# Kernel tuning notes

Measured on AMD Instinct MI355X. Metric: run time of the kernel, lower is better.

The kernel has to match this reference:

```python
import jax, jax.numpy as jnp
import numpy as np
from jax import lax


def conv1x1(x, w, b):
    # x [B,Ci,H,W], w [Co,Ci], b [Co]
    return jnp.einsum('oi,bihw->bohw', w, x) + b[None, :, None, None]


def dil_conv_relu(x, w, b):
    # 3x3 conv, dilation 2, padding 2 (make_layers with dilation=True), then ReLU
    y = lax.conv_general_dilated(x, w, (1, 1), [(2, 2), (2, 2)], rhs_dilation=(2, 2),
                                 dimension_numbers=('NCHW', 'OIHW', 'NCHW'))
    return jax.nn.relu(y + b[None, :, None, None])


def conv1d_relu(x, w, b):
    # x [n,c,L], w [o,i,9], padding 4 -> same length; conv + ReLU (nn.Sequential(Conv2d, ReLU))
    y = lax.conv_general_dilated(x, w, (1,), [(4, 4)], dimension_numbers=('NCH', 'OIH', 'NCH'))
    return jax.nn.relu(y + b[None, :, None])


def dulr_pass(slices, w, b):
    # slices [L,n,c,m]; out[0]=slices[0]; out[i]=convrelu(out[i-1]) + slices[i]
    def step(carry, s):
        new = conv1d_relu(carry, w, b) + s
        return new, new
    _, rest = lax.scan(step, slices[0], slices[1:])
    return jnp.concatenate([slices[:1], rest], axis=0)


def conv_du(x, w, b):
    # down pass then up pass over rows (kernel (1,9) -> 1D conv along width)
    rows = jnp.moveaxis(x, 2, 0)            # [h,n,c,w]
    rows = dulr_pass(rows, w, b)
    rows = dulr_pass(rows[::-1], w, b)[::-1]
    return jnp.moveaxis(rows, 0, 2)


def conv_lr(x, w, b):
    # left-right then right-left over columns (kernel (9,1) -> 1D conv along height)
    cols = jnp.moveaxis(x, 3, 0)            # [w,n,c,h]
    cols = dulr_pass(cols, w, b)
    cols = dulr_pass(cols[::-1], w, b)[::-1]
    return jnp.moveaxis(cols, 0, 3)


def setup_inputs() -> dict:
    key = jax.random.key(0)
    ks = jax.random.split(key, 24)
    B, H, W = 4, 64, 64
    std = 0.01
    f32 = jnp.float32
    d = {}
    d['in_data'] = jax.random.normal(ks[0], (B, 1025, H, W), f32)
    d['wA'] = jax.random.normal(ks[1], (128, 1024), f32) * std
    d['bA'] = jax.random.normal(ks[2], (128,), f32) * std
    d['wB'] = jax.random.normal(ks[3], (128, 1024), f32) * std
    d['bB'] = jax.random.normal(ks[4], (128,), f32) * std
    d['wC'] = jax.random.normal(ks[5], (1024, 1024), f32) * std
    d['bC'] = jax.random.normal(ks[6], (1024,), f32) * std
    d['gamma'] = jnp.array(0.1, f32)
    chans = [(512, 1024), (512, 512), (512, 512), (256, 512), (128, 256), (64, 128)]
    for i, (co, ci) in enumerate(chans):
        d[f'bw{i+1}'] = jax.random.normal(ks[7 + 2 * i], (co, ci, 3, 3), f32) * std
        d[f'bb{i+1}'] = jax.random.normal(ks[8 + 2 * i], (co,), f32) * std
    d['du_w'] = jax.random.normal(ks[19], (64, 64, 9), f32) * std
    d['du_b'] = jax.random.normal(ks[20], (64,), f32) * std
    d['lr_w'] = jax.random.normal(ks[21], (64, 64, 9), f32) * std
    d['lr_b'] = jax.random.normal(ks[22], (64,), f32) * std
    d['ow'] = jax.random.normal(ks[23], (1, 64), f32) * std
    d['ob'] = jnp.zeros((1,), f32)
    return d


def reference(in_data, wA, bA, wB, bB, wC, bC, gamma,
              bw1, bb1, bw2, bb2, bw3, bb3, bw4, bb4, bw5, bb5, bw6, bb6,
              du_w, du_b, lr_w, lr_b, ow, ob):
    x = in_data[:, :1024]                   # [B,1024,H,W]
    f = in_data[:, 1024:1025]               # [B,1,H,W]
    B, C, H, W = x.shape
    N = H * W
    # appearance_A(x) -> query [B,128,N]
    q = conv1x1(x, wA, bA).reshape(B, 128, N)
    # f1024 = f broadcast to 1024 channels; flow_B(f1024) (1x1 conv) == f * sum_i wB[:,i] + bB
    k = (f * wB.sum(axis=1)[None, :, None, None] + bB[None, :, None, None]).reshape(B, 128, N)
    energy = jnp.einsum('bcn,bcm->bnm', q, k)           # [B,N,N] = q^T k
    att = jax.nn.softmax(energy, axis=-1)
    v = conv1x1(x, wC, bC).reshape(B, C, N)             # appearance_C
    out = jnp.einsum('bcj,bij->bci', v, att).reshape(B, C, H, W)  # bmm(v, att^T)
    x = gamma * out + x
    for w_, b_ in ((bw1, bb1), (bw2, bb2), (bw3, bb3), (bw4, bb4), (bw5, bb5), (bw6, bb6)):
        x = dil_conv_relu(x, w_, b_)
    x = conv_du(x, du_w, du_b)
    x = conv_lr(x, lr_w, lr_b)
    x = jax.nn.relu(conv1x1(x, ow, ob))                 # o_layer
    # F.upsample(scale_factor=8) default nearest
    x = jnp.repeat(jnp.repeat(x, 8, axis=2), 8, axis=3)
    return x
```

## Files before the change

kernel.cpp:

```cpp
#include <hip/hip_runtime.h>


#define NPIX 4096

typedef _Float16 f16;
typedef _Float16 f16x8 __attribute__((ext_vector_type(8)));
typedef _Float16 f16x4 __attribute__((ext_vector_type(4)));
typedef float f32x4 __attribute__((ext_vector_type(4)));

__device__ inline void async16(const void* g, void* l) {
  __builtin_amdgcn_global_load_lds(
      (const __attribute__((address_space(1))) unsigned int*)g,
      (__attribute__((address_space(3))) unsigned int*)l, 16, 0, 0);
}


__global__ void rf_zero(float* __restrict__ z) { z[threadIdx.x] = 0.f; }

__global__ void rf_s(const float* __restrict__ wB, const float* __restrict__ bA,
                     float* __restrict__ s_out, float* __restrict__ c0_out) {
  int c = threadIdx.x;
  const float* row = wB + (size_t)c * 1024;
  float acc = 0.f;
  for (int i = 0; i < 1024; ++i) acc += row[i];
  s_out[c] = acc;
  __shared__ float sh[128];
  sh[c] = acc * bA[c];
  __syncthreads();
  for (int off = 64; off > 0; off >>= 1) {
    if (c < off) sh[c] += sh[c + off];
    __syncthreads();
  }
  if (c == 0) c0_out[0] = sh[0];
}

__global__ void rf_u(const float* __restrict__ wA, const float* __restrict__ s,
                     float* __restrict__ u) {
  int i = blockIdx.x * 256 + threadIdx.x;
  float acc = 0.f;
  for (int c = 0; c < 128; ++c) acc += s[c] * wA[(size_t)c * 1024 + i];
  u[i] = acc;
}

__global__ void rf_fstat(const float* __restrict__ in, float* __restrict__ fstat) {
  int b = blockIdx.x;
  int t = threadIdx.x;
  const float* f = in + ((size_t)b * 1025 + 1024) * NPIX;
  float mx = -1e30f, mn = 1e30f;
  for (int j = t; j < NPIX; j += 256) {
    float v = f[j];
    mx = fmaxf(mx, v);
    mn = fminf(mn, v);
  }
  __shared__ float smx[256], smn[256];
  smx[t] = mx; smn[t] = mn;
  __syncthreads();
  for (int off = 128; off > 0; off >>= 1) {
    if (t < off) {
      smx[t] = fmaxf(smx[t], smx[t + off]);
      smn[t] = fminf(smn[t], smn[t + off]);
    }
    __syncthreads();
  }
  if (t == 0) { fstat[b] = smx[0]; fstat[4 + b] = smn[0]; }
}

__global__ __launch_bounds__(256) void rf_A(const float* __restrict__ in,
                                            const float* __restrict__ u,
                                            const float* __restrict__ c0p,
                                            const float* __restrict__ fst,
                                            float* __restrict__ A, float* __restrict__ M) {
  __shared__ float ul[1024];
  int b = blockIdx.y;
  int n = blockIdx.x * 256 + threadIdx.x;
  for (int s = threadIdx.x; s < 1024; s += 256) ul[s] = u[s];
  __syncthreads();
  const float* xp = in + (size_t)b * 1025 * NPIX + n;
  float acc = c0p[0];
#pragma unroll 8
  for (int i = 0; i < 1024; ++i) acc = fmaf(ul[i], xp[(size_t)i * NPIX], acc);
  A[b * NPIX + n] = acc;
  M[b * NPIX + n] = fmaxf(acc * fst[b], acc * fst[4 + b]);
}

__global__ void rf_Z(const float* __restrict__ in, const float* __restrict__ A,
                     const float* __restrict__ M, float* __restrict__ iZ) {
  int idx = blockIdx.x * 4 + (threadIdx.x >> 6);
  int lane = threadIdx.x & 63;
  int b = idx >> 12;
  const float* f = in + ((size_t)b * 1025 + 1024) * NPIX;
  float a = A[idx], m = M[idx];
  float acc = 0.f;
#pragma unroll 4
  for (int it = 0; it < 64; ++it) acc += __expf(a * f[lane + it * 64] - m);
  for (int off = 32; off > 0; off >>= 1) acc += __shfl_down(acc, off, 64);
  if (lane == 0) iZ[idx] = 1.0f / acc;
}


__global__ void rf_xsplit(const float* __restrict__ in, f16* __restrict__ xh) {
  __shared__ float tl[64][65];
  int nt = blockIdx.x, ct = blockIdx.y, b = blockIdx.z;
  int n0 = nt * 64, c0 = ct * 64;
  int tid = threadIdx.x;
  for (int s = tid; s < 4096; s += 256) {
    int r = s >> 6, c = s & 63;
    tl[r][c] = in[((size_t)b * 1025 + c0 + r) * NPIX + n0 + c];
  }
  __syncthreads();
  for (int s = tid; s < 512; s += 256) {
    int n = s >> 3, g = s & 7;
    f16x8 hb;
#pragma unroll
    for (int q = 0; q < 8; ++q) hb[q] = (f16)(16.f * tl[g * 8 + q][n]);
    size_t o = ((size_t)b * NPIX + n0 + n) * 1024 + c0 + g * 8;
    *(f16x8*)&xh[o] = hb;
  }
}


__global__ void rf_wC1(const float* __restrict__ wC, f16* __restrict__ wh) {
  int base = (blockIdx.x * 256 + threadIdx.x) * 8;
  f16x8 hb;
#pragma unroll
  for (int q = 0; q < 8; ++q) hb[q] = (f16)(256.f * wC[base + q]);
  *(f16x8*)&wh[base] = hb;
}


__global__ __launch_bounds__(256, 2) void rf_vgemmm(
    const f16* __restrict__ wh, const f16* __restrict__ xh,
    const float* __restrict__ bC, f16* __restrict__ vH) {
  __shared__ f16 sA[2][4096], sB[2][4096];
  const int tid = threadIdx.x;
  const int nb = blockIdx.x * 128, cb = blockIdx.y * 128, b = blockIdx.z;
  const int pA = tid & 127;
  const int wv = tid >> 6, lane = tid & 63;
  const int mrow = lane & 15, quad = lane >> 4;
  const int wm = (wv & 1) * 64, wn = (wv >> 1) * 64;
  const size_t abase = (size_t)(cb + pA) * 1024;
  const size_t bbase = ((size_t)b * NPIX + nb + pA) * 1024;
  f32x4 acc[4][4];
#pragma unroll
  for (int i = 0; i < 4; ++i)
#pragma unroll
    for (int j = 0; j < 4; ++j) acc[i][j] = (f32x4){0.f, 0.f, 0.f, 0.f};

  auto stage = [&](int k0, int pb) {
#pragma unroll
    for (int s = 0; s < 2; ++s) {
      const int cc = ((tid + 256 * s) >> 7) & 3;
      const int lb = ((tid & ~63) + 256 * s) * 8;
      async16(wh + abase + k0 + cc * 8, &sA[pb][lb]);
      async16(xh + bbase + k0 + cc * 8, &sB[pb][lb]);
    }
  };
  stage(0, 0);
  int p = 0;
  for (int k0 = 0; k0 < 1024; k0 += 32) {
    __syncthreads();
    if (k0 + 32 < 1024) stage(k0 + 32, p ^ 1);
    f16x8 fa[4], fb[4];
#pragma unroll
    for (int mi = 0; mi < 4; ++mi)
      fa[mi] = *(const f16x8*)&sA[p][(quad * 128 + wm + mi * 16 + mrow) * 8];
#pragma unroll
    for (int ni = 0; ni < 4; ++ni)
      fb[ni] = *(const f16x8*)&sB[p][(quad * 128 + wn + ni * 16 + mrow) * 8];
#pragma unroll
    for (int mi = 0; mi < 4; ++mi)
#pragma unroll
      for (int ni = 0; ni < 4; ++ni)
        acc[mi][ni] = __builtin_amdgcn_mfma_f32_16x16x32_f16(fa[mi], fb[ni], acc[mi][ni], 0, 0, 0);
    p ^= 1;
  }
  const float inv = 1.0f / 4096.0f;
#pragma unroll
  for (int mi = 0; mi < 4; ++mi) {
#pragma unroll
    for (int rg = 0; rg < 4; ++rg) {
      int c = cb + wm + mi * 16 + quad * 4 + rg;
      float bv = bC[c];
#pragma unroll
      for (int ni = 0; ni < 4; ++ni) {
        int j = nb + wn + ni * 16 + mrow;
        vH[((size_t)b * 1024 + c) * NPIX + j] =
            (f16)(16.f * (acc[mi][ni][rg] * inv + bv));
      }
    }
  }
}


__global__ __launch_bounds__(256, 2) void rf_attm(
    const f16* __restrict__ vH,
    const float* __restrict__ Aarr, const float* __restrict__ Marr,
    const float* __restrict__ iZ, const float* __restrict__ in,
    const float* __restrict__ gptr, f16* __restrict__ yH) {
  __shared__ f16 sAh[3][8192];
  __shared__ f16 sPh[2][4096];
  __shared__ float fl[4096];
  const int tid = threadIdx.x;
  const int ib = blockIdx.x * 128, cb = blockIdx.y * 256, b = blockIdx.z;
  const int wv = tid >> 6, lane = tid & 63;
  const int mrow = lane & 15, quad = lane >> 4;
  const int wm = wv * 64;
  const int ni_ = tid & 127;
  const int kc0 = tid >> 7;
  const float av2 = Aarr[b * NPIX + ib + ni_] * 1.44269504f;
  const float mv2 = Marr[b * NPIX + ib + ni_] * 1.44269504f;
  const float* f = in + ((size_t)b * 1025 + 1024) * NPIX;
  const f16* vrow = vH + ((size_t)b * 1024 + cb + tid) * NPIX;

  f32x4 acc[4][8];
#pragma unroll
  for (int i = 0; i < 4; ++i)
#pragma unroll
    for (int j = 0; j < 8; ++j) acc[i][j] = (f32x4){0.f, 0.f, 0.f, 0.f};

  auto stage = [&](int j0, int pb) {
#pragma unroll
    for (int s = 0; s < 4; ++s)
      async16(vrow + j0 + s * 8, &sAh[pb][(s * 256 + tid) * 8]);
  };
  auto doP = [&](int j0, int pb) {
#pragma unroll
    for (int it = 0; it < 2; ++it) {
      const int kc = kc0 + 2 * it;
      const float4 fa4 = *(const float4*)&fl[j0 + kc * 8];
      const float4 fb4 = *(const float4*)&fl[j0 + kc * 8 + 4];
      const float fj[8] = {fa4.x, fa4.y, fa4.z, fa4.w, fb4.x, fb4.y, fb4.z, fb4.w};
      f16x8 ph;
#pragma unroll
      for (int q = 0; q < 8; ++q)
        ph[q] = (f16)exp2f(fmaf(av2, fj[q], -mv2));
      *(f16x8*)&sPh[pb][(kc * 128 + ni_) * 8] = ph;
    }
  };

#pragma unroll
  for (int s = 0; s < 4; ++s)
    async16(f + (tid + 256 * s) * 4, &fl[((tid & ~63) + 256 * s) * 4]);
  stage(0, 0);
  asm volatile("s_waitcnt vmcnt(0)" ::: "memory");
  __builtin_amdgcn_s_barrier();
  doP(0, 0);
  stage(32, 1);
  asm volatile("s_waitcnt lgkmcnt(0)" ::: "memory");
  __builtin_amdgcn_s_barrier();

  for (int k = 0; k < 126; ++k) {
    const int pa = k % 3;
    const int pp = k & 1;
    f16x8 fa[4], fb[8];
#pragma unroll
    for (int mi = 0; mi < 4; ++mi)
      fa[mi] = *(const f16x8*)&sAh[pa][(quad * 256 + wm + mi * 16 + mrow) * 8];
#pragma unroll
    for (int ni = 0; ni < 8; ++ni)
      fb[ni] = *(const f16x8*)&sPh[pp][(quad * 128 + ni * 16 + mrow) * 8];
    stage((k + 2) * 32, (k + 2) % 3);
    doP((k + 1) * 32, pp ^ 1);
#pragma unroll
    for (int mi = 0; mi < 4; ++mi)
#pragma unroll
      for (int ni = 0; ni < 8; ++ni)
        acc[mi][ni] = __builtin_amdgcn_mfma_f32_16x16x32_f16(fa[mi], fb[ni], acc[mi][ni], 0, 0, 0);
    asm volatile("s_waitcnt vmcnt(4) lgkmcnt(0)" ::: "memory");
    __builtin_amdgcn_s_barrier();
  }
  {
    f16x8 fa[4], fb[8];
#pragma unroll
    for (int mi = 0; mi < 4; ++mi)
      fa[mi] = *(const f16x8*)&sAh[0][(quad * 256 + wm + mi * 16 + mrow) * 8];
#pragma unroll
    for (int ni = 0; ni < 8; ++ni)
      fb[ni] = *(const f16x8*)&sPh[0][(quad * 128 + ni * 16 + mrow) * 8];
    doP(127 * 32, 1);
#pragma unroll
    for (int mi = 0; mi < 4; ++mi)
#pragma unroll
      for (int ni = 0; ni < 8; ++ni)
        acc[mi][ni] = __builtin_amdgcn_mfma_f32_16x16x32_f16(fa[mi], fb[ni], acc[mi][ni], 0, 0, 0);
    asm volatile("s_waitcnt vmcnt(0) lgkmcnt(0)" ::: "memory");
    __builtin_amdgcn_s_barrier();
  }
  {
    f16x8 fa[4], fb[8];
#pragma unroll
    for (int mi = 0; mi < 4; ++mi)
      fa[mi] = *(const f16x8*)&sAh[1][(quad * 256 + wm + mi * 16 + mrow) * 8];
#pragma unroll
    for (int ni = 0; ni < 8; ++ni)
      fb[ni] = *(const f16x8*)&sPh[1][(quad * 128 + ni * 16 + mrow) * 8];
#pragma unroll
    for (int mi = 0; mi < 4; ++mi)
#pragma unroll
      for (int ni = 0; ni < 8; ++ni)
        acc[mi][ni] = __builtin_amdgcn_mfma_f32_16x16x32_f16(fa[mi], fb[ni], acc[mi][ni], 0, 0, 0);
  }

  const float g = gptr[0];
  const float inv16 = 1.0f / 16.0f;
  float zvi[8];
#pragma unroll
  for (int ni = 0; ni < 8; ++ni)
    zvi[ni] = iZ[b * NPIX + ib + ni * 16 + mrow] * inv16;
#pragma unroll
  for (int mi = 0; mi < 4; ++mi) {
    const int cbase = cb + wm + mi * 16 + quad * 4;
#pragma unroll
    for (int ni = 0; ni < 8; ++ni) {
      const int i = ib + ni * 16 + mrow;
      f16x4 hv;
#pragma unroll
      for (int rg = 0; rg < 4; ++rg) {
        float xr = in[((size_t)b * 1025 + cbase + rg) * NPIX + i];
        hv[rg] = (f16)(16.f * (g * (acc[mi][ni][rg] * zvi[ni]) + xr));
      }
      *(f16x4*)&yH[((size_t)b * NPIX + i) * 1024 + cbase] = hv;
    }
  }
}


__global__ void rf_wfragc(const float* __restrict__ w, f16* __restrict__ F,
                          int CI, int CO) {
  int gid = blockIdx.x * 256 + threadIdx.x;
  const int C16 = CO >> 4, KI = CI >> 5;
  const int total = 9 * KI * C16 * 64;
  if (gid >= total) return;
  int lane = gid & 63;
  int rest = gid >> 6;
  int c16 = rest % C16;
  int rest2 = rest / C16;
  int k = rest2 % KI;
  int t = rest2 / KI;
  int co = c16 * 16 + (lane & 15);
  int ci = k * 32 + (lane >> 4) * 8;
  f16x8 hb;
#pragma unroll
  for (int j = 0; j < 8; ++j)
    hb[j] = (f16)(256.0f * w[((size_t)co * CI + ci + j) * 9 + t]);
  *(f16x8*)&F[(size_t)gid * 8] = hb;
}


template <int BM, int BN, bool F32OUT>
__global__ __launch_bounds__(256, 2) void rf_mconv(
    const f16* __restrict__ xh, const f16* __restrict__ F,
    const float* __restrict__ bias, const float* __restrict__ zp,
    f16* __restrict__ oh, float* __restrict__ of, int CI, int CO) {
  constexpr int ROWS = BM / 64;
  constexpr int TPI = 4096 / BM;
  constexpr int HROWS = ROWS + 4;
  constexpr int COLP = 72;
  constexpr int CHUNKS = HROWS * 4 * COLP;
  constexpr int NSTG = (CHUNKS + 255) / 256;
  __shared__ f16 sA[2][NSTG * 2048];
  const int tid = threadIdx.x;
  const int blkpx = blockIdx.x;
  const int cob = blockIdx.y * BN;
  const int b = blkpx / TPI;
  const int h0 = (blkpx - b * TPI) * ROWS;

  const int wv = tid >> 6, lane = tid & 63;
  const int mrow = lane & 15, quad = lane >> 4;
  const int wm = (BN == 128) ? (wv & 1) * 64 : wv * 64;
  const int wn = (BN == 128) ? (wv >> 1) * 64 : 0;
  const int r_out = wm >> 6;
  const int KI = CI >> 5;
  const int C16 = CO >> 4;
  const int cb16 = (cob + wn) >> 4;

  f32x4 acc[4][4];
#pragma unroll
  for (int i = 0; i < 4; ++i)
#pragma unroll
    for (int j = 0; j < 4; ++j) acc[i][j] = (f32x4){0.f, 0.f, 0.f, 0.f};

  const f16* abase[NSTG];
  unsigned vmask = 0;
#pragma unroll
  for (int s = 0; s < NSTG; ++s) {
    int idx = tid + 256 * s;
    int rowks = idx / COLP;
    int col = idx - rowks * COLP;
    int r = rowks >> 2, ks = rowks & 3;
    int srow = h0 + r - 2, scol = col - 2;
    bool ok = (idx < CHUNKS) && ((unsigned)srow < 64u) && ((unsigned)scol < 64u);
    abase[s] = ok ? xh + (((size_t)b * 64 + srow) * 64 + scol) * CI + ks * 8
                  : (const f16*)zp;
    if (ok) vmask |= (1u << s);
  }
  auto stageA = [&](int k, int pb) {
#pragma unroll
    for (int s = 0; s < NSTG; ++s) {
      const f16* sp = abase[s] + (((vmask >> s) & 1u) ? k * 32 : 0);
      async16(sp, &sA[pb][((tid & ~63) + 256 * s) * 8]);
    }
  };

  const f16* Fb = F + ((size_t)cb16 * 64 + lane) * 8;

  stageA(0, 0);
  int p = 0;
  for (int k = 0; k < KI; ++k) {
    __syncthreads();
    if (k + 1 < KI) stageA(k + 1, p ^ 1);
#pragma unroll
    for (int t = 0; t < 9; ++t) {
      const int dh = (t / 3) * 2 - 2, dw = (t - (t / 3) * 3) * 2 - 2;
      f16x8 fb[4];
#pragma unroll
      for (int ni = 0; ni < 4; ++ni)
        fb[ni] = *(const f16x8*)(Fb + ((size_t)(t * KI + k) * C16 + ni) * 512);
      f16x8 fa[4];
#pragma unroll
      for (int mi = 0; mi < 4; ++mi)
        fa[mi] = *(const f16x8*)&sA[p][(((r_out + dh + 2) * 4 + quad) * COLP +
                                       mi * 16 + mrow + dw + 2) * 8];
#pragma unroll
      for (int mi = 0; mi < 4; ++mi)
#pragma unroll
        for (int ni = 0; ni < 4; ++ni)
          acc[mi][ni] = __builtin_amdgcn_mfma_f32_16x16x32_f16(fa[mi], fb[ni], acc[mi][ni], 0, 0, 0);
    }
    p ^= 1;
  }

  const float inv = 1.0f / 4096.0f;
  float bvs[4];
#pragma unroll
  for (int ni = 0; ni < 4; ++ni) bvs[ni] = bias[cob + wn + ni * 16 + mrow];
#pragma unroll
  for (int mi = 0; mi < 4; ++mi) {
#pragma unroll
    for (int rg = 0; rg < 4; ++rg) {
      int px = wm + mi * 16 + quad * 4 + rg;
      int hh = h0 + (px >> 6), wwp = px & 63;
#pragma unroll
      for (int ni = 0; ni < 4; ++ni) {
        int co = cob + wn + ni * 16 + mrow;
        float vv = fmaxf(acc[mi][ni][rg] * inv + bvs[ni], 0.f);
        if (F32OUT) {
          of[(((size_t)b * CO + co) * 64 + hh) * 64 + wwp] = vv;
        } else {
          oh[(((size_t)b * 64 + hh) * 64 + wwp) * CO + co] = (f16)(vv * 16.f);
        }
      }
    }
  }
}


__global__ void rf_wfrag(const float* __restrict__ w, f16* __restrict__ fh) {
  int gid = blockIdx.x * 256 + threadIdx.x;
  if (gid >= 4608) return;
  int lane = gid & 63;
  int rem = gid >> 6;
  int kc = rem & 1;
  int rem2 = rem >> 1;
  int t = rem2 % 9;
  int w4 = rem2 / 9;
  int co = w4 * 16 + (lane & 15);
  int cib = kc * 32 + (lane >> 4) * 8;
  f16x8 hb;
#pragma unroll
  for (int j = 0; j < 8; ++j)
    hb[j] = (f16)(256.f * w[((size_t)co * 64 + cib + j) * 9 + t]);
  *(f16x8*)&fh[(size_t)gid * 8] = hb;
}


__global__ __launch_bounds__(256, 1) void rf_mscan(
    const float* __restrict__ src, float* __restrict__ dst,
    const f16* __restrict__ fh, const float* __restrict__ bias, int dir) {
  __shared__ f16 ch[72 * 64];
  const int b = blockIdx.x;
  const int tid = threadIdx.x;
  const int wave = tid >> 6, lane = tid & 63;
  const int quad = lane >> 4, l15 = lane & 15;

  f16x8 Ah[9][2];
#pragma unroll
  for (int t = 0; t < 9; ++t)
#pragma unroll
    for (int kc = 0; kc < 2; ++kc)
      Ah[t][kc] = *(const f16x8*)&fh[(((wave * 9 + t) * 2 + kc) * 64 + lane) * 8];
  float bvs[4];
#pragma unroll
  for (int r = 0; r < 4; ++r) bvs[r] = bias[wave * 16 + quad * 4 + r];

  for (int s = tid; s < 2304; s += 256) ((unsigned*)ch)[s] = 0u;
  __syncthreads();

  const size_t sbase = (size_t)b * 64 * 4096;
  const int row0 = (dir > 0) ? 0 : 63;
  {
    int pos0 = tid & 63, cig = tid >> 6;
#pragma unroll
    for (int q = 0; q < 16; ++q) {
      int ci = cig * 16 + q;
      float v = src[sbase + (size_t)ci * 4096 + row0 * 64 + pos0];
      dst[sbase + (size_t)ci * 4096 + row0 * 64 + pos0] = v;
      int rowIdx = pos0 + 4;
      ch[rowIdx * 64 + (((ci >> 3) ^ (rowIdx & 7)) << 3) + (ci & 7)] = (f16)v;
    }
  }
  __syncthreads();

  const float inv = 1.0f / 256.0f;
  for (int s = 1; s < 64; ++s) {
    const int row = (dir > 0) ? s : 63 - s;
    float srow[4][4];
#pragma unroll
    for (int nt = 0; nt < 4; ++nt)
#pragma unroll
      for (int r = 0; r < 4; ++r)
        srow[nt][r] = src[sbase + (size_t)(wave * 16 + quad * 4 + r) * 4096 +
                          row * 64 + nt * 16 + l15];
    f32x4 acc[4];
#pragma unroll
    for (int nt = 0; nt < 4; ++nt) acc[nt] = (f32x4){0.f, 0.f, 0.f, 0.f};
#pragma unroll
    for (int t = 0; t < 9; ++t)
#pragma unroll
      for (int kc = 0; kc < 2; ++kc) {
#pragma unroll
        for (int nt = 0; nt < 4; ++nt) {
          int rowIdx = nt * 16 + l15 + t;
          int gr = kc * 4 + quad;
          f16x8 Bh = *(const f16x8*)&ch[rowIdx * 64 + ((gr ^ (rowIdx & 7)) << 3)];
          acc[nt] = __builtin_amdgcn_mfma_f32_16x16x32_f16(Ah[t][kc], Bh, acc[nt], 0, 0, 0);
        }
      }
    __syncthreads();
#pragma unroll
    for (int nt = 0; nt < 4; ++nt) {
      int pos = nt * 16 + l15;
      int rowIdx = pos + 4;
      f16x4 hv;
#pragma unroll
      for (int r = 0; r < 4; ++r) {
        float v = fmaxf(acc[nt][r] * inv + bvs[r], 0.f) + srow[nt][r];
        dst[sbase + (size_t)(wave * 16 + quad * 4 + r) * 4096 + row * 64 + pos] = v;
        hv[r] = (f16)v;
      }
      int ci0 = wave * 16 + quad * 4;
      *(f16x4*)&ch[rowIdx * 64 + (((ci0 >> 3) ^ (rowIdx & 7)) << 3) + (ci0 & 7)] = hv;
    }
    __syncthreads();
  }
}


__global__ void rf_transpose(const float* __restrict__ src, float* __restrict__ dst) {
  int bc = blockIdx.x;
  __shared__ float tl[64][65];
  int tid = threadIdx.x;
  const float* sp = src + (size_t)bc * 4096;
  float* dp = dst + (size_t)bc * 4096;
  for (int s = tid; s < 4096; s += 256) {
    int h = s >> 6, w = s & 63;
    tl[w][h] = sp[s];
  }
  __syncthreads();
  for (int s = tid; s < 4096; s += 256) dp[s] = tl[s >> 6][s & 63];
}


__global__ void rf_final(const float* __restrict__ t, const float* __restrict__ ow,
                         const float* __restrict__ ob, float* __restrict__ out) {
  int b = blockIdx.y;
  int s = blockIdx.x * 256 + threadIdx.x;
  int w = s >> 6, h = s & 63;
  float acc = ob[0];
  for (int c = 0; c < 64; ++c)
    acc += ow[c] * t[(((size_t)b * 64 + c) * 64 + w) * 64 + h];
  acc = fmaxf(acc, 0.f);
  float4 vv = make_float4(acc, acc, acc, acc);
  for (int dy = 0; dy < 8; ++dy) {
    float* dp = out + ((size_t)b * 512 + h * 8 + dy) * 512 + w * 8;
    *(float4*)dp = vv;
    *(float4*)(dp + 4) = vv;
  }
}


extern "C" void kernel_launch(void* const* d_in, const int* in_sizes, int n_in,
                              void* d_out, int out_size, void* d_ws, size_t ws_size,
                              hipStream_t stream) {
  const float* in    = (const float*)d_in[0];
  const float* wA    = (const float*)d_in[1];
  const float* bA    = (const float*)d_in[2];
  const float* wB    = (const float*)d_in[3];
  const float* wC    = (const float*)d_in[5];
  const float* bC    = (const float*)d_in[6];
  const float* gamma = (const float*)d_in[7];
  const float* bw1 = (const float*)d_in[8];  const float* bb1 = (const float*)d_in[9];
  const float* bw2 = (const float*)d_in[10]; const float* bb2 = (const float*)d_in[11];
  const float* bw3 = (const float*)d_in[12]; const float* bb3 = (const float*)d_in[13];
  const float* bw4 = (const float*)d_in[14]; const float* bb4 = (const float*)d_in[15];
  const float* bw5 = (const float*)d_in[16]; const float* bb5 = (const float*)d_in[17];
  const float* bw6 = (const float*)d_in[18]; const float* bb6 = (const float*)d_in[19];
  const float* du_w = (const float*)d_in[20]; const float* du_b = (const float*)d_in[21];
  const float* lr_w = (const float*)d_in[22]; const float* lr_b = (const float*)d_in[23];
  const float* ow   = (const float*)d_in[24]; const float* ob   = (const float*)d_in[25];
  float* out = (float*)d_out;
  float* ws = (float*)d_ws;

  f16* vH  = (f16*)(ws + 0);
  f16* xTh = (f16*)(ws + 4194304);
  f16* wCh = (f16*)(ws + 8388608);
  f16* yH  = (f16*)(ws + 16777216);
  f16* w1h = (f16*)(ws + 0);
  f16* c1H = (f16*)(ws + 2359296);
  f16* w3h = (f16*)(ws + 6553600);
  f16* w2h = (f16*)(ws + 16777216);
  f16* c2H = (f16*)(ws + 17956864);
  f16* w4h = (f16*)(ws + 22151168);
  f16* c4H = (f16*)(ws + 22740992);
  f16* c3H = c1H;
  f16* w5h = (f16*)(ws + 0);
  f16* c5H = (f16*)(ws + 147456);
  f16* w6h = (f16*)(ws + 1196032);
  float* tin = ws + 1232896;
  float* t0  = ws + 2281472;
  float* t1  = ws + 3330048;
  f16* duFh = (f16*)(ws + 4378624);
  f16* lrFh = (f16*)(ws + 4397056);
  float* sm = ws + 33554432;
  float* A_  = sm;
  float* M_  = sm + 16384;
  float* iZ  = sm + 32768;
  float* u_  = sm + 49152;
  float* s_  = sm + 50176;
  float* c0_ = sm + 50304;
  float* fst = sm + 50308;
  float* zp  = sm + 50432;

  rf_zero<<<1, 64, 0, stream>>>(zp);
  rf_s<<<1, 128, 0, stream>>>(wB, bA, s_, c0_);
  rf_u<<<4, 256, 0, stream>>>(wA, s_, u_);
  rf_fstat<<<4, 256, 0, stream>>>(in, fst);
  rf_A<<<dim3(16, 4), 256, 0, stream>>>(in, u_, c0_, fst, A_, M_);
  rf_Z<<<4096, 256, 0, stream>>>(in, A_, M_, iZ);
  rf_xsplit<<<dim3(64, 16, 4), 256, 0, stream>>>(in, xTh);
  rf_wC1<<<512, 256, 0, stream>>>(wC, wCh);
  rf_vgemmm<<<dim3(32, 8, 4), 256, 0, stream>>>(wCh, xTh, bC, vH);
  rf_attm<<<dim3(32, 4, 4), 256, 0, stream>>>(vH, A_, M_, iZ, in, gamma, yH);

  rf_wfragc<<<2304, 256, 0, stream>>>(bw1, w1h, 1024, 512);
  rf_wfragc<<<1152, 256, 0, stream>>>(bw3, w3h, 512, 512);
  rf_mconv<128, 128, false><<<dim3(128, 4), 256, 0, stream>>>(
      yH, w1h, bb1, zp, c1H, nullptr, 1024, 512);
  rf_wfragc<<<1152, 256, 0, stream>>>(bw2, w2h, 512, 512);
  rf_wfragc<<<576, 256, 0, stream>>>(bw4, w4h, 512, 256);
  rf_wfragc<<<144, 256, 0, stream>>>(bw5, w5h, 256, 128);
  rf_wfragc<<<36, 256, 0, stream>>>(bw6, w6h, 128, 64);
  rf_mconv<128, 128, false><<<dim3(128, 4), 256, 0, stream>>>(
      c1H, w2h, bb2, zp, c2H, nullptr, 512, 512);
  rf_mconv<128, 128, false><<<dim3(128, 4), 256, 0, stream>>>(
      c2H, w3h, bb3, zp, c3H, nullptr, 512, 512);
  rf_mconv<128, 128, false><<<dim3(128, 2), 256, 0, stream>>>(
      c3H, w4h, bb4, zp, c4H, nullptr, 512, 256);
  rf_wfrag<<<18, 256, 0, stream>>>(du_w, duFh);
  rf_wfrag<<<18, 256, 0, stream>>>(lr_w, lrFh);
  rf_mconv<128, 128, false><<<dim3(128, 1), 256, 0, stream>>>(
      c4H, w5h, bb5, zp, c5H, nullptr, 256, 128);
  rf_mconv<256, 64, true><<<dim3(64, 1), 256, 0, stream>>>(
      c5H, w6h, bb6, zp, nullptr, tin, 128, 64);

  rf_mscan<<<4, 256, 0, stream>>>(tin, t0, duFh, du_b, +1);
  rf_mscan<<<4, 256, 0, stream>>>(t0, t1, duFh, du_b, -1);
  rf_transpose<<<256, 256, 0, stream>>>(t1, t0);
  rf_mscan<<<4, 256, 0, stream>>>(t0, t1, lrFh, lr_b, +1);
  rf_mscan<<<4, 256, 0, stream>>>(t1, t0, lrFh, lr_b, -1);
  rf_final<<<dim3(16, 4), 256, 0, stream>>>(t0, ow, ob, out);
}
```

Before: 1.683 ms.

## Prefetch conv weight fragments one tap ahead and remap blocks across XCDs

The dilated-conv MFMA kernel now double-buffers its global weight-fragment loads in registers, loading the next tap's fragments while the current tap's MFMAs run. It also moves the activation staging for the next K-step to after the compute, and unrolls the K loop by two so the buffer indices are compile-time. Separately, the 2D grid becomes a 1D grid whose block index is remapped so that blocks sharing the same output-channel tile land on the same XCD, aiming at better L2 reuse of weights. The changes raise register pressure. The unrolled K loop assumes KI is even.

```diff
diff --git a/kernel.cpp b/kernel.cpp
--- a/kernel.cpp
+++ b/kernel.cpp
@@ -351,7 +351,7 @@
 __global__ __launch_bounds__(256, 2) void rf_mconv(
     const f16* __restrict__ xh, const f16* __restrict__ F,
     const float* __restrict__ bias, const float* __restrict__ zp,
-    f16* __restrict__ oh, float* __restrict__ of, int CI, int CO) {
+    f16* __restrict__ oh, float* __restrict__ of, int CI, int CO, int NCB) {
   constexpr int ROWS = BM / 64;
   constexpr int TPI = 4096 / BM;
   constexpr int HROWS = ROWS + 4;
@@ -360,10 +360,14 @@
   constexpr int NSTG = (CHUNKS + 255) / 256;
   __shared__ f16 sA[2][NSTG * 2048];
   const int tid = threadIdx.x;
-  const int blkpx = blockIdx.x;
-  const int cob = blockIdx.y * BN;
-  const int b = blkpx / TPI;
-  const int h0 = (blkpx - b * TPI) * ROWS;
+  const int bid = blockIdx.x;
+  const int R8 = 8 / NCB;
+  const int xcd = bid & 7;
+  const int cobi = xcd / R8;
+  const int pxi = (bid >> 3) * R8 + (xcd % R8);
+  const int cob = cobi * BN;
+  const int b = pxi / TPI;
+  const int h0 = (pxi - b * TPI) * ROWS;
 
   const int wv = tid >> 6, lane = tid & 63;
   const int mrow = lane & 15, quad = lane >> 4;
@@ -403,31 +407,42 @@
   };
 
   const f16* Fb = F + ((size_t)cb16 * 64 + lane) * 8;
+  auto loadFB = [&](f16x8* dst, int t, int k) {
+#pragma unroll
+    for (int ni = 0; ni < 4; ++ni)
+      dst[ni] = *(const f16x8*)(Fb + ((size_t)(t * KI + k) * C16 + ni) * 512);
+  };
 
   stageA(0, 0);
-  int p = 0;
-  for (int k = 0; k < KI; ++k) {
-    __syncthreads();
-    if (k + 1 < KI) stageA(k + 1, p ^ 1);
-#pragma unroll
-    for (int t = 0; t < 9; ++t) {
-      const int dh = (t / 3) * 2 - 2, dw = (t - (t / 3) * 3) * 2 - 2;
-      f16x8 fb[4];
-#pragma unroll
-      for (int ni = 0; ni < 4; ++ni)
-        fb[ni] = *(const f16x8*)(Fb + ((size_t)(t * KI + k) * C16 + ni) * 512);
-      f16x8 fa[4];
-#pragma unroll
-      for (int mi = 0; mi < 4; ++mi)
-        fa[mi] = *(const f16x8*)&sA[p][(((r_out + dh + 2) * 4 + quad) * COLP +
-                                       mi * 16 + mrow + dw + 2) * 8];
-#pragma unroll
-      for (int mi = 0; mi < 4; ++mi)
-#pragma unroll
-        for (int ni = 0; ni < 4; ++ni)
-          acc[mi][ni] = __builtin_amdgcn_mfma_f32_16x16x32_f16(fa[mi], fb[ni], acc[mi][ni], 0, 0, 0);
-    }
-    p ^= 1;
+  f16x8 fb0[4], fb1[4];
+  loadFB(fb0, 0, 0);
+
+  for (int k2 = 0; k2 < KI; k2 += 2) {
+#pragma unroll
+    for (int dk = 0; dk < 2; ++dk) {
+      const int k = k2 + dk;
+      __syncthreads();
+#pragma unroll
+      for (int t = 0; t < 9; ++t) {
+        const int par = (t + dk) & 1;
+        f16x8* cur = par ? fb1 : fb0;
+        f16x8* nxt = par ? fb0 : fb1;
+        if (t < 8) loadFB(nxt, t + 1, k);
+        else if (k + 1 < KI) loadFB(nxt, 0, k + 1);
+        const int dh = (t / 3) * 2 - 2, dw = (t - (t / 3) * 3) * 2 - 2;
+        f16x8 fa[4];
+#pragma unroll
+        for (int mi = 0; mi < 4; ++mi)
+          fa[mi] = *(const f16x8*)&sA[dk][(((r_out + dh + 2) * 4 + quad) * COLP +
+                                          mi * 16 + mrow + dw + 2) * 8];
+#pragma unroll
+        for (int mi = 0; mi < 4; ++mi)
+#pragma unroll
+          for (int ni = 0; ni < 4; ++ni)
+            acc[mi][ni] = __builtin_amdgcn_mfma_f32_16x16x32_f16(fa[mi], cur[ni], acc[mi][ni], 0, 0, 0);
+      }
+      if (k + 1 < KI) stageA(k + 1, dk ^ 1);
+    }
   }
 
   const float inv = 1.0f / 4096.0f;
@@ -654,24 +669,24 @@
 
   rf_wfragc<<<2304, 256, 0, stream>>>(bw1, w1h, 1024, 512);
   rf_wfragc<<<1152, 256, 0, stream>>>(bw3, w3h, 512, 512);
-  rf_mconv<128, 128, false><<<dim3(128, 4), 256, 0, stream>>>(
-      yH, w1h, bb1, zp, c1H, nullptr, 1024, 512);
+  rf_mconv<128, 128, false><<<512, 256, 0, stream>>>(
+      yH, w1h, bb1, zp, c1H, nullptr, 1024, 512, 4);
   rf_wfragc<<<1152, 256, 0, stream>>>(bw2, w2h, 512, 512);
   rf_wfragc<<<576, 256, 0, stream>>>(bw4, w4h, 512, 256);
   rf_wfragc<<<144, 256, 0, stream>>>(bw5, w5h, 256, 128);
   rf_wfragc<<<36, 256, 0, stream>>>(bw6, w6h, 128, 64);
-  rf_mconv<128, 128, false><<<dim3(128, 4), 256, 0, stream>>>(
-      c1H, w2h, bb2, zp, c2H, nullptr, 512, 512);
-  rf_mconv<128, 128, false><<<dim3(128, 4), 256, 0, stream>>>(
-      c2H, w3h, bb3, zp, c3H, nullptr, 512, 512);
-  rf_mconv<128, 128, false><<<dim3(128, 2), 256, 0, stream>>>(
-      c3H, w4h, bb4, zp, c4H, nullptr, 512, 256);
+  rf_mconv<128, 128, false><<<512, 256, 0, stream>>>(
+      c1H, w2h, bb2, zp, c2H, nullptr, 512, 512, 4);
+  rf_mconv<128, 128, false><<<512, 256, 0, stream>>>(
+      c2H, w3h, bb3, zp, c3H, nullptr, 512, 512, 4);
+  rf_mconv<128, 128, false><<<256, 256, 0, stream>>>(
+      c3H, w4h, bb4, zp, c4H, nullptr, 512, 256, 2);
   rf_wfrag<<<18, 256, 0, stream>>>(du_w, duFh);
   rf_wfrag<<<18, 256, 0, stream>>>(lr_w, lrFh);
-  rf_mconv<128, 128, false><<<dim3(128, 1), 256, 0, stream>>>(
-      c4H, w5h, bb5, zp, c5H, nullptr, 256, 128);
-  rf_mconv<256, 64, true><<<dim3(64, 1), 256, 0, stream>>>(
-      c5H, w6h, bb6, zp, nullptr, tin, 128, 64);
+  rf_mconv<128, 128, false><<<128, 256, 0, stream>>>(
+      c4H, w5h, bb5, zp, c5H, nullptr, 256, 128, 1);
+  rf_mconv<256, 64, true><<<64, 256, 0, stream>>>(
+      c5H, w6h, bb6, zp, nullptr, tin, 128, 64, 1);
 
   rf_mscan<<<4, 256, 0, stream>>>(tin, t0, duFh, du_b, +1);
   rf_mscan<<<4, 256, 0, stream>>>(t0, t1, duFh, du_b, -1);
```

Result: no change. 1.680 ms (-0.2%).

## Switch f16 activations to channel-blocked layout and double-buffer conv weight fragments

Applied to the files above, without the earlier changes.

Every f16 intermediate (x, wC, v, y, conv outputs) moves from pixel-major rows of 1024 channels to a blocked [C/8][pixel][8] layout. The aim is for neighbouring threads in the async 16-byte LDS loads to read contiguous memory instead of rows strided by the channel count. The producer, GEMM, attention and dilated-conv kernels all change their index math to match. The dilated conv loop also prefetches the next tap's weight fragments into registers and issues the next A-stage after compute. This raises register pressure and relies on KI being even.

```diff
diff --git a/kernel.cpp b/kernel.cpp
--- a/kernel.cpp
+++ b/kernel.cpp
@@ -113,7 +113,7 @@
     f16x8 hb;
 #pragma unroll
     for (int q = 0; q < 8; ++q) hb[q] = (f16)(16.f * tl[g * 8 + q][n]);
-    size_t o = ((size_t)b * NPIX + n0 + n) * 1024 + c0 + g * 8;
+    size_t o = (((size_t)b * 128 + (c0 >> 3) + g) * 4096 + n0 + n) * 8;
     *(f16x8*)&xh[o] = hb;
   }
 }
@@ -121,10 +121,11 @@
 
 __global__ void rf_wC1(const float* __restrict__ wC, f16* __restrict__ wh) {
   int base = (blockIdx.x * 256 + threadIdx.x) * 8;
+  int c = base >> 10, i0 = base & 1023;
   f16x8 hb;
 #pragma unroll
   for (int q = 0; q < 8; ++q) hb[q] = (f16)(256.f * wC[base + q]);
-  *(f16x8*)&wh[base] = hb;
+  *(f16x8*)&wh[(((size_t)(i0 >> 3)) * 1024 + c) * 8] = hb;
 }
 
 
@@ -138,8 +139,6 @@
   const int wv = tid >> 6, lane = tid & 63;
   const int mrow = lane & 15, quad = lane >> 4;
   const int wm = (wv & 1) * 64, wn = (wv >> 1) * 64;
-  const size_t abase = (size_t)(cb + pA) * 1024;
-  const size_t bbase = ((size_t)b * NPIX + nb + pA) * 1024;
   f32x4 acc[4][4];
 #pragma unroll
   for (int i = 0; i < 4; ++i)
@@ -147,12 +146,13 @@
     for (int j = 0; j < 4; ++j) acc[i][j] = (f32x4){0.f, 0.f, 0.f, 0.f};
 
   auto stage = [&](int k0, int pb) {
+    const int kg = k0 >> 3;
 #pragma unroll
     for (int s = 0; s < 2; ++s) {
       const int cc = ((tid + 256 * s) >> 7) & 3;
       const int lb = ((tid & ~63) + 256 * s) * 8;
-      async16(wh + abase + k0 + cc * 8, &sA[pb][lb]);
-      async16(xh + bbase + k0 + cc * 8, &sB[pb][lb]);
+      async16(wh + ((size_t)(kg + cc) * 1024 + cb + pA) * 8, &sA[pb][lb]);
+      async16(xh + (((size_t)b * 128 + kg + cc) * 4096 + nb + pA) * 8, &sB[pb][lb]);
     }
   };
   stage(0, 0);
@@ -184,7 +184,7 @@
 #pragma unroll
       for (int ni = 0; ni < 4; ++ni) {
         int j = nb + wn + ni * 16 + mrow;
-        vH[((size_t)b * 1024 + c) * NPIX + j] =
+        vH[(((size_t)b * 512 + (j >> 3)) * 1024 + c) * 8 + (j & 7)] =
             (f16)(16.f * (acc[mi][ni][rg] * inv + bv));
       }
     }
@@ -210,7 +210,7 @@
   const float av2 = Aarr[b * NPIX + ib + ni_] * 1.44269504f;
   const float mv2 = Marr[b * NPIX + ib + ni_] * 1.44269504f;
   const float* f = in + ((size_t)b * 1025 + 1024) * NPIX;
-  const f16* vrow = vH + ((size_t)b * 1024 + cb + tid) * NPIX;
+  const f16* vbase = vH + (size_t)b * 4194304 + ((size_t)cb + tid) * 8;
 
   f32x4 acc[4][8];
 #pragma unroll
@@ -219,9 +219,10 @@
     for (int j = 0; j < 8; ++j) acc[i][j] = (f32x4){0.f, 0.f, 0.f, 0.f};
 
   auto stage = [&](int j0, int pb) {
+    const int jg = j0 >> 3;
 #pragma unroll
     for (int s = 0; s < 4; ++s)
-      async16(vrow + j0 + s * 8, &sAh[pb][(s * 256 + tid) * 8]);
+      async16(vbase + (size_t)(jg + s) * 8192, &sAh[pb][(s * 256 + tid) * 8]);
   };
   auto doP = [&](int j0, int pb) {
 #pragma unroll
@@ -319,7 +320,7 @@
         float xr = in[((size_t)b * 1025 + cbase + rg) * NPIX + i];
         hv[rg] = (f16)(16.f * (g * (acc[mi][ni][rg] * zvi[ni]) + xr));
       }
-      *(f16x4*)&yH[((size_t)b * NPIX + i) * 1024 + cbase] = hv;
+      *(f16x4*)&yH[(((size_t)b * 128 + (cbase >> 3)) * 4096 + i) * 8 + (cbase & 7)] = hv;
     }
   }
 }
@@ -390,44 +391,55 @@
     int r = rowks >> 2, ks = rowks & 3;
     int srow = h0 + r - 2, scol = col - 2;
     bool ok = (idx < CHUNKS) && ((unsigned)srow < 64u) && ((unsigned)scol < 64u);
-    abase[s] = ok ? xh + (((size_t)b * 64 + srow) * 64 + scol) * CI + ks * 8
+    abase[s] = ok ? xh + (((size_t)b * (CI >> 3) + ks) * 4096 + srow * 64 + scol) * 8
                   : (const f16*)zp;
     if (ok) vmask |= (1u << s);
   }
   auto stageA = [&](int k, int pb) {
 #pragma unroll
     for (int s = 0; s < NSTG; ++s) {
-      const f16* sp = abase[s] + (((vmask >> s) & 1u) ? k * 32 : 0);
+      const f16* sp = abase[s] + (((vmask >> s) & 1u) ? k * 131072 : 0);
       async16(sp, &sA[pb][((tid & ~63) + 256 * s) * 8]);
     }
   };
 
   const f16* Fb = F + ((size_t)cb16 * 64 + lane) * 8;
+  auto loadFB = [&](f16x8* dst, int t, int k) {
+#pragma unroll
+    for (int ni = 0; ni < 4; ++ni)
+      dst[ni] = *(const f16x8*)(Fb + ((size_t)(t * KI + k) * C16 + ni) * 512);
+  };
 
   stageA(0, 0);
-  int p = 0;
-  for (int k = 0; k < KI; ++k) {
-    __syncthreads();
-    if (k + 1 < KI) stageA(k + 1, p ^ 1);
-#pragma unroll
-    for (int t = 0; t < 9; ++t) {
-      const int dh = (t / 3) * 2 - 2, dw = (t - (t / 3) * 3) * 2 - 2;
-      f16x8 fb[4];
-#pragma unroll
-      for (int ni = 0; ni < 4; ++ni)
-        fb[ni] = *(const f16x8*)(Fb + ((size_t)(t * KI + k) * C16 + ni) * 512);
-      f16x8 fa[4];
-#pragma unroll
-      for (int mi = 0; mi < 4; ++mi)
-        fa[mi] = *(const f16x8*)&sA[p][(((r_out + dh + 2) * 4 + quad) * COLP +
-                                       mi * 16 + mrow + dw + 2) * 8];
-#pragma unroll
-      for (int mi = 0; mi < 4; ++mi)
-#pragma unroll
-        for (int ni = 0; ni < 4; ++ni)
-          acc[mi][ni] = __builtin_amdgcn_mfma_f32_16x16x32_f16(fa[mi], fb[ni], acc[mi][ni], 0, 0, 0);
-    }
-    p ^= 1;
+  f16x8 fb0[4], fb1[4];
+  loadFB(fb0, 0, 0);
+
+  for (int k2 = 0; k2 < KI; k2 += 2) {
+#pragma unroll
+    for (int dk = 0; dk < 2; ++dk) {
+      const int k = k2 + dk;
+      __syncthreads();
+#pragma unroll
+      for (int t = 0; t < 9; ++t) {
+        const int par = (t + dk) & 1;
+        f16x8* cur = par ? fb1 : fb0;
+        f16x8* nxt = par ? fb0 : fb1;
+        if (t < 8) loadFB(nxt, t + 1, k);
+        else if (k + 1 < KI) loadFB(nxt, 0, k + 1);
+        const int dh = (t / 3) * 2 - 2, dw = (t - (t / 3) * 3) * 2 - 2;
+        f16x8 fa[4];
+#pragma unroll
+        for (int mi = 0; mi < 4; ++mi)
+          fa[mi] = *(const f16x8*)&sA[dk][(((r_out + dh + 2) * 4 + quad) * COLP +
+                                          mi * 16 + mrow + dw + 2) * 8];
+#pragma unroll
+        for (int mi = 0; mi < 4; ++mi)
+#pragma unroll
+          for (int ni = 0; ni < 4; ++ni)
+            acc[mi][ni] = __builtin_amdgcn_mfma_f32_16x16x32_f16(fa[mi], cur[ni], acc[mi][ni], 0, 0, 0);
+      }
+      if (k + 1 < KI) stageA(k + 1, dk ^ 1);
+    }
   }
 
   const float inv = 1.0f / 4096.0f;
@@ -447,7 +459,8 @@
         if (F32OUT) {
           of[(((size_t)b * CO + co) * 64 + hh) * 64 + wwp] = vv;
         } else {
-          oh[(((size_t)b * 64 + hh) * 64 + wwp) * CO + co] = (f16)(vv * 16.f);
+          oh[(((size_t)b * (CO >> 3) + (co >> 3)) * 4096 + hh * 64 + wwp) * 8 + (co & 7)] =
+              (f16)(vv * 16.f);
         }
       }
     }
```

Measured after the change: 1.556 ms. -7.5%, faster.
